# Kernel tuning notes

Measured on AMD Instinct MI355X. Metric: run time of the kernel, lower is better.

Reference implementation:

```python
import jax, jax.numpy as jnp
import numpy as np
from functools import partial

IMG, P, DIM, DEPTH, HEADS, MLP = 224, 16, 768, 6, 12, 3072
N = (IMG // P) ** 2            # 196 patches
PIX = P * P * 3                # 768 pixel values per patch
RATIO = 0.5
NUM_MASKED = int(RATIO * N)    # 98


def patchify(img):
    # b (h p1) (w p2) c -> b (h w) (p1 p2 c)
    b, H, W, c = img.shape
    g = H // P
    x = img.reshape(b, g, P, g, P, c)
    x = x.transpose(0, 1, 3, 2, 4, 5)
    return x.reshape(b, g * g, P * P * c)


def layernorm(x, s, b, eps=1e-5):
    m = jnp.mean(x, axis=-1, keepdims=True)
    v = jnp.var(x, axis=-1, keepdims=True)
    return (x - m) * jax.lax.rsqrt(v + eps) * s + b


def setup_inputs() -> dict:
    key = jax.random.key(0)
    ks = jax.random.split(key, 16)
    B = 64
    s = 0.02
    inp = {
        "img": jax.random.normal(ks[0], (B, IMG, IMG, 3), jnp.float32),
        "mask_noise": jax.random.uniform(ks[1], (B, N), jnp.float32),
        "patch_w": jax.random.normal(ks[2], (PIX, DIM), jnp.float32) * s,
        "patch_b": jnp.zeros((DIM,), jnp.float32),
        "pos_emb": jax.random.normal(ks[3], (1, N + 1, DIM), jnp.float32) * s,
        "mask_token": jax.random.normal(ks[4], (DIM,), jnp.float32),
        "ln1_s": jnp.ones((DEPTH, DIM), jnp.float32),
        "ln1_b": jnp.zeros((DEPTH, DIM), jnp.float32),
        "wqkv": jax.random.normal(ks[5], (DEPTH, DIM, 3 * DIM), jnp.float32) * s,
        "bqkv": jnp.zeros((DEPTH, 3 * DIM), jnp.float32),
        "wo": jax.random.normal(ks[6], (DEPTH, DIM, DIM), jnp.float32) * s,
        "bo": jnp.zeros((DEPTH, DIM), jnp.float32),
        "ln2_s": jnp.ones((DEPTH, DIM), jnp.float32),
        "ln2_b": jnp.zeros((DEPTH, DIM), jnp.float32),
        "w1": jax.random.normal(ks[7], (DEPTH, DIM, MLP), jnp.float32) * s,
        "b1": jnp.zeros((DEPTH, MLP), jnp.float32),
        "w2": jax.random.normal(ks[8], (DEPTH, MLP, DIM), jnp.float32) * s,
        "b2": jnp.zeros((DEPTH, DIM), jnp.float32),
        "pix_w": jax.random.normal(ks[9], (DIM, PIX), jnp.float32) * s,
        "pix_b": jnp.zeros((PIX,), jnp.float32),
    }
    return inp


def transformer(tokens, ln1_s, ln1_b, wqkv, bqkv, wo, bo, ln2_s, ln2_b, w1, b1, w2, b2):
    dh = DIM // HEADS
    scale = 1.0 / jnp.sqrt(jnp.float32(dh))

    def layer(x, p):
        l1s, l1b, Wqkv, Bqkv, Wo, Bo, l2s, l2b, W1, B1, W2, B2 = p
        h = layernorm(x, l1s, l1b)
        qkv = h @ Wqkv + Bqkv                              # [b,n,3D]
        b, n, _ = qkv.shape
        q, k, v = jnp.split(qkv.reshape(b, n, 3, HEADS, dh), 3, axis=2)
        q, k, v = (t[:, :, 0] for t in (q, k, v))          # [b,n,h,d]
        attn = jax.nn.softmax(jnp.einsum('bqhd,bkhd->bhqk', q, k) * scale, axis=-1)
        out = jnp.einsum('bhqk,bkhd->bqhd', attn, v).reshape(b, n, DIM)
        x = x + out @ Wo + Bo
        h = layernorm(x, l2s, l2b)
        x = x + jax.nn.gelu(h @ W1 + B1) @ W2 + B2
        return x, None

    params = (ln1_s, ln1_b, wqkv, bqkv, wo, bo, ln2_s, ln2_b, w1, b1, w2, b2)
    x, _ = jax.lax.scan(layer, tokens, params)
    return x


def reference(img, mask_noise, patch_w, patch_b, pos_emb, mask_token,
              ln1_s, ln1_b, wqkv, bqkv, wo, bo, ln2_s, ln2_b, w1, b1, w2, b2,
              pix_w, pix_b):
    patches = patchify(img)                               # [B,N,PIX]
    B = patches.shape[0]
    batch_range = jnp.arange(B)[:, None]
    pe = pos_emb[:, 1:N + 1]                              # skip cls position

    tokens = patches @ patch_w + patch_b + pe             # [B,N,D]
    mask_tokens = mask_token + pe                         # [1,N,D] broadcast

    _, masked_indices = jax.lax.top_k(mask_noise, NUM_MASKED)   # [B,K]
    bool_mask = jnp.zeros((B, N), bool).at[batch_range, masked_indices].set(True)
    tokens = jnp.where(bool_mask[..., None], mask_tokens, tokens)

    encoded = transformer(tokens, ln1_s, ln1_b, wqkv, bqkv, wo, bo,
                          ln2_s, ln2_b, w1, b1, w2, b2)

    encoded_mask = encoded[batch_range, masked_indices]   # [B,K,D]
    pred = encoded_mask @ pix_w + pix_b                   # [B,K,PIX]
    masked_patches = patches[batch_range, masked_indices]
    recon_loss = jnp.mean(jnp.abs(pred - masked_patches)) / NUM_MASKED
    return recon_loss
```

## Files before the change

kernel.cpp:

```cpp
#include <hip/hip_runtime.h>
#include <hip/hip_bf16.h>
#include <math.h>

#define BATCH   64
#define NPATCH  196
#define DIM     768
#define DEPTH   6
#define HEADS   12
#define DHEAD   64
#define MLPDIM  3072
#define NMASK   98
#define TOKENS  (BATCH*NPATCH)
#define MROWS   (BATCH*NMASK)
#define HALFROWS (TOKENS/2)

using bf16_t = __hip_bfloat16;
typedef short bf16x8 __attribute__((ext_vector_type(8)));
typedef short short4v __attribute__((ext_vector_type(4)));
typedef float floatx4 __attribute__((ext_vector_type(4)));

__device__ inline float gelu_f(float v) {
    const float c = 0.7978845608028654f;
    float t = tanhf(c * (v + 0.044715f * v * v * v));
    return 0.5f * v * (1.0f + t);
}

__device__ __forceinline__ short f2bf_s(float f) {
    bf16_t t = __float2bfloat16(f);
    return *reinterpret_cast<short*>(&t);
}

__device__ __forceinline__ void gload_lds16(const bf16_t* g, bf16_t* l) {
    __builtin_amdgcn_global_load_lds(
        (const __attribute__((address_space(1))) unsigned int*)g,
        (__attribute__((address_space(3))) unsigned int*)l, 16, 0, 0);
}

__device__ __forceinline__ int xcd_swz(int orig, int nwg) {
    const int qq = nwg >> 3, rr = nwg & 7;
    const int xcd = orig & 7, seq = orig >> 3;
    return (xcd < rr ? xcd * (qq + 1) : rr * (qq + 1) + (xcd - rr) * qq) + seq;
}

template<int MODE>
__global__ __launch_bounds__(256) void mm_bf16(
    const bf16_t* __restrict__ A, const bf16_t* __restrict__ BT,
    const float* __restrict__ bias, const float* __restrict__ Cin,
    void* __restrict__ Cout, int M, int N, int K)
{
    __shared__ __align__(16) bf16_t As[128 * 64];
    __shared__ __align__(16) bf16_t Bs[128 * 64];

    const int tid  = threadIdx.x;
    const int lane = tid & 63;
    const int wave = tid >> 6;
    const int wm = (wave >> 1) * 64;
    const int wn = (wave & 1) * 64;

    const int gx  = gridDim.x;
    const int wg = xcd_swz(blockIdx.y * gx + blockIdx.x, gx * gridDim.y);
    const int m0 = (wg / gx) * 128;
    const int n0 = (wg % gx) * 128;

    const int srow = tid >> 3;
    const int schunk = (tid & 7) ^ (srow & 7);
    const bf16_t* gA = A  + (size_t)(m0 + srow) * K + schunk * 8;
    const bf16_t* gB = BT + (size_t)(n0 + srow) * K + schunk * 8;
    bf16_t* lA = &As[tid * 8];
    bf16_t* lB = &Bs[tid * 8];

    floatx4 acc[4][4];
#pragma unroll
    for (int i = 0; i < 4; ++i)
#pragma unroll
        for (int j = 0; j < 4; ++j) acc[i][j] = (floatx4)0.0f;

    const int quad = lane >> 4;
    const int rm = lane & 15;

    for (int k0 = 0; k0 < K; k0 += 64) {
        __syncthreads();
#pragma unroll
        for (int i = 0; i < 4; ++i) {
            gload_lds16(gA + k0 + (size_t)(32 * i) * K, lA + i * 2048);
            gload_lds16(gB + k0 + (size_t)(32 * i) * K, lB + i * 2048);
        }
        __syncthreads();

#pragma unroll
        for (int kk = 0; kk < 2; ++kk) {
            const int kq = (((kk << 2) | quad) ^ (rm & 7)) * 8;
            bf16x8 a[4], b[4];
#pragma unroll
            for (int mi = 0; mi < 4; ++mi)
                a[mi] = *(const bf16x8*)&As[(wm + mi * 16 + rm) * 64 + kq];
#pragma unroll
            for (int ni = 0; ni < 4; ++ni)
                b[ni] = *(const bf16x8*)&Bs[(wn + ni * 16 + rm) * 64 + kq];
#pragma unroll
            for (int mi = 0; mi < 4; ++mi)
#pragma unroll
                for (int ni = 0; ni < 4; ++ni)
                    acc[mi][ni] = __builtin_amdgcn_mfma_f32_16x16x32_bf16(
                        a[mi], b[ni], acc[mi][ni], 0, 0, 0);
        }
    }

    const int cm = m0 + wm + quad * 4;
    const int cn = n0 + wn + rm;
#pragma unroll
    for (int mi = 0; mi < 4; ++mi) {
#pragma unroll
        for (int ni = 0; ni < 4; ++ni) {
#pragma unroll
            for (int r = 0; r < 4; ++r) {
                const int row = cm + mi * 16 + r;
                const int col = cn + ni * 16;
                float v = acc[mi][ni][r] + bias[col];
                const size_t idx = (size_t)row * N + col;
                if (MODE == 0) {
                    ((float*)Cout)[idx] = v;
                } else if (MODE == 1) {
                    ((bf16_t*)Cout)[idx] = __float2bfloat16(gelu_f(v));
                } else if (MODE == 2) {
                    ((float*)Cout)[idx] = v + Cin[idx];
                } else {
                    ((bf16_t*)Cout)[idx] = __float2bfloat16(v);
                }
            }
        }
    }
}

template<int MODE>
__global__ __launch_bounds__(256) void mm64_bf16(
    const bf16_t* __restrict__ A, const bf16_t* __restrict__ BT,
    const float* __restrict__ bias, const float* __restrict__ Cin,
    void* __restrict__ Cout, int M, int N, int K)
{
    __shared__ __align__(16) bf16_t As[64 * 64];
    __shared__ __align__(16) bf16_t Bs[64 * 64];

    const int tid  = threadIdx.x;
    const int lane = tid & 63;
    const int wave = tid >> 6;
    const int wm = (wave >> 1) * 32;
    const int wn = (wave & 1) * 32;

    const int gx  = gridDim.x;
    const int wg = xcd_swz(blockIdx.y * gx + blockIdx.x, gx * gridDim.y);
    const int m0 = (wg / gx) * 64;
    const int n0 = (wg % gx) * 64;

    const int srow = tid >> 3;
    const int schunk = (tid & 7) ^ (srow & 7);
    const bf16_t* gA = A  + (size_t)(m0 + srow) * K + schunk * 8;
    const bf16_t* gB = BT + (size_t)(n0 + srow) * K + schunk * 8;
    bf16_t* lA = &As[tid * 8];
    bf16_t* lB = &Bs[tid * 8];

    floatx4 acc[2][2];
#pragma unroll
    for (int i = 0; i < 2; ++i)
#pragma unroll
        for (int j = 0; j < 2; ++j) acc[i][j] = (floatx4)0.0f;

    const int quad = lane >> 4;
    const int rm = lane & 15;

    for (int k0 = 0; k0 < K; k0 += 64) {
        __syncthreads();
#pragma unroll
        for (int i = 0; i < 2; ++i) {
            gload_lds16(gA + k0 + (size_t)(32 * i) * K, lA + i * 2048);
            gload_lds16(gB + k0 + (size_t)(32 * i) * K, lB + i * 2048);
        }
        __syncthreads();

#pragma unroll
        for (int kk = 0; kk < 2; ++kk) {
            const int kq = (((kk << 2) | quad) ^ (rm & 7)) * 8;
            bf16x8 a[2], b[2];
#pragma unroll
            for (int mi = 0; mi < 2; ++mi)
                a[mi] = *(const bf16x8*)&As[(wm + mi * 16 + rm) * 64 + kq];
#pragma unroll
            for (int ni = 0; ni < 2; ++ni)
                b[ni] = *(const bf16x8*)&Bs[(wn + ni * 16 + rm) * 64 + kq];
#pragma unroll
            for (int mi = 0; mi < 2; ++mi)
#pragma unroll
                for (int ni = 0; ni < 2; ++ni)
                    acc[mi][ni] = __builtin_amdgcn_mfma_f32_16x16x32_bf16(
                        a[mi], b[ni], acc[mi][ni], 0, 0, 0);
        }
    }

    const int cm = m0 + wm + quad * 4;
    const int cn = n0 + wn + rm;
#pragma unroll
    for (int mi = 0; mi < 2; ++mi) {
#pragma unroll
        for (int ni = 0; ni < 2; ++ni) {
#pragma unroll
            for (int r = 0; r < 4; ++r) {
                const int row = cm + mi * 16 + r;
                const int col = cn + ni * 16;
                float v = acc[mi][ni][r] + bias[col];
                const size_t idx = (size_t)row * N + col;
                if (MODE == 0) {
                    ((float*)Cout)[idx] = v;
                } else if (MODE == 1) {
                    ((bf16_t*)Cout)[idx] = __float2bfloat16(gelu_f(v));
                } else if (MODE == 2) {
                    ((float*)Cout)[idx] = v + Cin[idx];
                } else {
                    ((bf16_t*)Cout)[idx] = __float2bfloat16(v);
                }
            }
        }
    }
}

__global__ __launch_bounds__(256) void wconvT(
    const float* __restrict__ W, bf16_t* __restrict__ WT, int K, int N)
{
    __shared__ float t[32][33];
    const size_t off = (size_t)blockIdx.z * K * N;
    const int k0 = blockIdx.y * 32, n0 = blockIdx.x * 32;
    const int r = threadIdx.x >> 5, c = threadIdx.x & 31;
#pragma unroll
    for (int i = 0; i < 4; ++i)
        t[r + i * 8][c] = W[off + (size_t)(k0 + r + i * 8) * N + n0 + c];
    __syncthreads();
#pragma unroll
    for (int i = 0; i < 4; ++i)
        WT[off + (size_t)(n0 + r + i * 8) * K + k0 + c] =
            __float2bfloat16(t[c][r + i * 8]);
}

__global__ __launch_bounds__(256) void patchify_kernel(
    const float* __restrict__ img, bf16_t* __restrict__ patches)
{
    const int row = blockIdx.x;
    const int b = row / NPATCH, p = row % NPATCH;
    const int gy = p / 14, gx = p % 14;
    for (int e = threadIdx.x; e < 768; e += 256) {
        const int c = e % 3, pix = e / 3;
        const int py = pix / 16, px = pix % 16;
        const size_t src = (((size_t)b * 224 + gy * 16 + py) * 224 + gx * 16 + px) * 3 + c;
        patches[(size_t)row * 768 + e] = __float2bfloat16(img[src]);
    }
}

__global__ __launch_bounds__(256) void mask_kernel(
    const float* __restrict__ noise, int* __restrict__ flags, int* __restrict__ midx)
{
    const int b = blockIdx.x;
    __shared__ float v[NPATCH];
    const int t = threadIdx.x;
    if (t < NPATCH) v[t] = noise[b * NPATCH + t];
    __syncthreads();
    if (t < NPATCH) {
        const float mine = v[t];
        int r = 0;
        for (int j = 0; j < NPATCH; ++j) {
            const float o = v[j];
            r += (o > mine) || (o == mine && j < t);
        }
        const int f = (r < NMASK) ? 1 : 0;
        flags[b * NPATCH + t] = f;
        if (f) midx[b * NMASK + r] = t;
    }
}

__global__ __launch_bounds__(256) void pe_mask_kernel(
    float* __restrict__ x, const float* __restrict__ pos_emb,
    const float* __restrict__ mask_token, const int* __restrict__ flags)
{
    const int wave = threadIdx.x >> 6, lane = threadIdx.x & 63;
    const int row = blockIdx.x * 4 + wave;
    const int n = row % NPATCH;
    const int masked = flags[row];
    const float* pe = pos_emb + (size_t)(n + 1) * 768;
    float* xr = x + (size_t)row * 768;
#pragma unroll
    for (int j = 0; j < 3; ++j) {
        const int off = j * 256 + lane * 4;
        const float4 pev = *(const float4*)(pe + off);
        float4 o;
        if (masked) {
            const float4 mt = *(const float4*)(mask_token + off);
            o.x = mt.x + pev.x; o.y = mt.y + pev.y;
            o.z = mt.z + pev.z; o.w = mt.w + pev.w;
        } else {
            const float4 xv = *(const float4*)(xr + off);
            o.x = xv.x + pev.x; o.y = xv.y + pev.y;
            o.z = xv.z + pev.z; o.w = xv.w + pev.w;
        }
        *(float4*)(xr + off) = o;
    }
}

__global__ __launch_bounds__(256) void ln_kernel(
    const float* __restrict__ x, bf16_t* __restrict__ out,
    const float* __restrict__ s, const float* __restrict__ bvec)
{
    const int wave = threadIdx.x >> 6, lane = threadIdx.x & 63;
    const int row = blockIdx.x * 4 + wave;
    const float* xr = x + (size_t)row * 768;

    float4 v[3];
    float sum = 0.0f, sq = 0.0f;
#pragma unroll
    for (int j = 0; j < 3; ++j) {
        v[j] = *(const float4*)(xr + j * 256 + lane * 4);
        sum += v[j].x + v[j].y + v[j].z + v[j].w;
        sq  += v[j].x * v[j].x + v[j].y * v[j].y + v[j].z * v[j].z + v[j].w * v[j].w;
    }
#pragma unroll
    for (int off = 32; off; off >>= 1) {
        sum += __shfl_xor(sum, off, 64);
        sq  += __shfl_xor(sq, off, 64);
    }
    const float mean = sum * (1.0f / 768.0f);
    const float var = sq * (1.0f / 768.0f) - mean * mean;
    const float inv = rsqrtf(var + 1e-5f);

    bf16_t* orow = out + (size_t)row * 768;
#pragma unroll
    for (int j = 0; j < 3; ++j) {
        const int off = j * 256 + lane * 4;
        const float4 sv = *(const float4*)(s + off);
        const float4 bv = *(const float4*)(bvec + off);
        short4v o;
        o[0] = f2bf_s((v[j].x - mean) * inv * sv.x + bv.x);
        o[1] = f2bf_s((v[j].y - mean) * inv * sv.y + bv.y);
        o[2] = f2bf_s((v[j].z - mean) * inv * sv.z + bv.z);
        o[3] = f2bf_s((v[j].w - mean) * inv * sv.w + bv.w);
        *(short4v*)(orow + off) = o;
    }
}

__global__ __launch_bounds__(256) void attn_kernel(
    const bf16_t* __restrict__ qkv, bf16_t* __restrict__ out)
{
    const int bh = blockIdx.x;
    const int b = bh / HEADS, h = bh % HEADS;
    const int tid = threadIdx.x, lane = tid & 63, wave = tid >> 6;
    const int quad = lane >> 4, l16 = lane & 15;
    const int wq = wave * 64;

    __shared__ __align__(16) short Vt[64][68];
    __shared__ __align__(16) short Plds[4][64][68];
    __shared__ float red[4][64];

    const size_t tok0 = (size_t)b * NPATCH;
    const int hoff = h * 64;

    bf16x8 qf[4][2];
#pragma unroll
    for (int ni = 0; ni < 4; ++ni) {
        const int q = wq + ni * 16 + l16;
        const int qe = q < 195 ? q : 195;
#pragma unroll
        for (int ks = 0; ks < 2; ++ks)
            qf[ni][ks] = *(const bf16x8*)(qkv + (tok0 + qe) * 2304 + hoff + ks * 32 + quad * 8);
    }

    floatx4 accO[4][4];
#pragma unroll
    for (int i = 0; i < 4; ++i)
#pragma unroll
        for (int j = 0; j < 4; ++j) accO[i][j] = (floatx4)0.0f;
    float mrun[4], lrun[4];
#pragma unroll
    for (int ni = 0; ni < 4; ++ni) { mrun[ni] = -1e30f; lrun[ni] = 0.0f; }

    for (int kc = 0; kc < 256; kc += 64) {
        __syncthreads();
        {
            const int kl = tid & 63;
            const int dg = tid >> 6;
            const int key = kc + kl;
            if (key < NPATCH) {
                const bf16_t* src = qkv + (tok0 + key) * 2304 + 1536 + hoff + dg * 16;
                bf16x8 v0 = *(const bf16x8*)src;
                bf16x8 v1 = *(const bf16x8*)(src + 8);
#pragma unroll
                for (int j = 0; j < 8; ++j) {
                    Vt[dg * 16 + j][kl]     = v0[j];
                    Vt[dg * 16 + 8 + j][kl] = v1[j];
                }
            } else {
#pragma unroll
                for (int j = 0; j < 16; ++j) Vt[dg * 16 + j][kl] = 0;
            }
        }
        __syncthreads();

        bf16x8 af[4][2];
#pragma unroll
        for (int mi = 0; mi < 4; ++mi) {
            const int key = kc + mi * 16 + l16;
            const int ke = key < 195 ? key : 195;
#pragma unroll
            for (int ks = 0; ks < 2; ++ks)
                af[mi][ks] = *(const bf16x8*)(qkv + (tok0 + ke) * 2304 + 768 + hoff + ks * 32 + quad * 8);
        }
        floatx4 accS[4][4];
#pragma unroll
        for (int i = 0; i < 4; ++i)
#pragma unroll
            for (int j = 0; j < 4; ++j) accS[i][j] = (floatx4)0.0f;
#pragma unroll
        for (int mi = 0; mi < 4; ++mi)
#pragma unroll
            for (int ni = 0; ni < 4; ++ni)
#pragma unroll
                for (int ks = 0; ks < 2; ++ks)
                    accS[mi][ni] = __builtin_amdgcn_mfma_f32_16x16x32_bf16(
                        af[mi][ks], qf[ni][ks], accS[mi][ni], 0, 0, 0);

#pragma unroll
        for (int mi = 0; mi < 4; ++mi) {
#pragma unroll
            for (int r = 0; r < 4; ++r) {
                const int key = kc + mi * 16 + quad * 4 + r;
                const bool valid = key < NPATCH;
#pragma unroll
                for (int ni = 0; ni < 4; ++ni)
                    accS[mi][ni][r] = valid ? accS[mi][ni][r] * 0.125f : -1e30f;
            }
        }

        float alpha[4];
#pragma unroll
        for (int ni = 0; ni < 4; ++ni) {
            float mx = -1e30f;
#pragma unroll
            for (int mi = 0; mi < 4; ++mi)
#pragma unroll
                for (int r = 0; r < 4; ++r) mx = fmaxf(mx, accS[mi][ni][r]);
            mx = fmaxf(mx, __shfl_xor(mx, 16, 64));
            mx = fmaxf(mx, __shfl_xor(mx, 32, 64));
            const float mnew = fmaxf(mrun[ni], mx);
            float s = 0.0f;
#pragma unroll
            for (int mi = 0; mi < 4; ++mi)
#pragma unroll
                for (int r = 0; r < 4; ++r) {
                    const float p = __expf(accS[mi][ni][r] - mnew);
                    accS[mi][ni][r] = p;
                    s += p;
                }
            s += __shfl_xor(s, 16, 64);
            s += __shfl_xor(s, 32, 64);
            alpha[ni] = __expf(mrun[ni] - mnew);
            lrun[ni] = lrun[ni] * alpha[ni] + s;
            mrun[ni] = mnew;
        }
        if (quad == 0) {
#pragma unroll
            for (int ni = 0; ni < 4; ++ni) red[wave][ni * 16 + l16] = alpha[ni];
        }

#pragma unroll
        for (int mi = 0; mi < 4; ++mi)
#pragma unroll
            for (int ni = 0; ni < 4; ++ni) {
                short4v pk;
#pragma unroll
                for (int r = 0; r < 4; ++r) pk[r] = f2bf_s(accS[mi][ni][r]);
                *(short4v*)&Plds[wave][ni * 16 + l16][mi * 16 + quad * 4] = pk;
            }
        asm volatile("s_waitcnt lgkmcnt(0)" ::: "memory");

#pragma unroll
        for (int mi = 0; mi < 4; ++mi) {
            const float4 al = *(const float4*)&red[wave][mi * 16 + quad * 4];
#pragma unroll
            for (int ni = 0; ni < 4; ++ni) {
                accO[mi][ni][0] *= al.x;
                accO[mi][ni][1] *= al.y;
                accO[mi][ni][2] *= al.z;
                accO[mi][ni][3] *= al.w;
            }
        }

#pragma unroll
        for (int ks = 0; ks < 2; ++ks) {
            bf16x8 pa[4], vb[4];
#pragma unroll
            for (int mi = 0; mi < 4; ++mi) {
                short4v lo = *(const short4v*)&Plds[wave][mi * 16 + l16][ks * 32 + quad * 8];
                short4v hi = *(const short4v*)&Plds[wave][mi * 16 + l16][ks * 32 + quad * 8 + 4];
                pa[mi] = __builtin_shufflevector(lo, hi, 0, 1, 2, 3, 4, 5, 6, 7);
            }
#pragma unroll
            for (int ni = 0; ni < 4; ++ni) {
                short4v lo = *(const short4v*)&Vt[ni * 16 + l16][ks * 32 + quad * 8];
                short4v hi = *(const short4v*)&Vt[ni * 16 + l16][ks * 32 + quad * 8 + 4];
                vb[ni] = __builtin_shufflevector(lo, hi, 0, 1, 2, 3, 4, 5, 6, 7);
            }
#pragma unroll
            for (int mi = 0; mi < 4; ++mi)
#pragma unroll
                for (int ni = 0; ni < 4; ++ni)
                    accO[mi][ni] = __builtin_amdgcn_mfma_f32_16x16x32_bf16(
                        pa[mi], vb[ni], accO[mi][ni], 0, 0, 0);
        }
    }

    if (quad == 0) {
#pragma unroll
        for (int ni = 0; ni < 4; ++ni) red[wave][ni * 16 + l16] = lrun[ni];
    }
    asm volatile("s_waitcnt lgkmcnt(0)" ::: "memory");
#pragma unroll
    for (int mi = 0; mi < 4; ++mi) {
        const float4 lv = *(const float4*)&red[wave][mi * 16 + quad * 4];
        const float inv[4] = {1.0f / lv.x, 1.0f / lv.y, 1.0f / lv.z, 1.0f / lv.w};
#pragma unroll
        for (int r = 0; r < 4; ++r) {
            const int q = wq + mi * 16 + quad * 4 + r;
            if (q < NPATCH) {
#pragma unroll
                for (int ni = 0; ni < 4; ++ni) {
                    const int d = ni * 16 + l16;
                    out[(tok0 + q) * 768 + hoff + d] =
                        __float2bfloat16(accO[mi][ni][r] * inv[r]);
                }
            }
        }
    }
}

__global__ __launch_bounds__(256) void gather_kernel(
    const float* __restrict__ x, const int* __restrict__ midx, bf16_t* __restrict__ em)
{
    const int row = blockIdx.x;
    const int b = row / NMASK;
    const int n = midx[row];
    const float* src = x + (size_t)(b * NPATCH + n) * 768;
    bf16_t* dst = em + (size_t)row * 768;
    for (int e = threadIdx.x; e < 768; e += 256) dst[e] = __float2bfloat16(src[e]);
}

__global__ void zero_kernel(float* __restrict__ p) {
    if (threadIdx.x == 0 && blockIdx.x == 0) p[0] = 0.0f;
}

__global__ __launch_bounds__(256) void loss_kernel(
    const float* __restrict__ pred, const float* __restrict__ img,
    const int* __restrict__ midx, float* __restrict__ acc)
{
    const size_t total = (size_t)MROWS * 768;
    float part = 0.0f;
    for (size_t idx = (size_t)blockIdx.x * blockDim.x + threadIdx.x; idx < total;
         idx += (size_t)gridDim.x * blockDim.x) {
        const int e = (int)(idx % 768);
        const int row = (int)(idx / 768);
        const int b = row / NMASK;
        const int n = midx[row];
        const int c = e % 3, pix = e / 3;
        const int py = pix / 16, px = pix % 16;
        const int gy = n / 14, gx = n % 14;
        const float ref =
            img[(((size_t)b * 224 + gy * 16 + py) * 224 + gx * 16 + px) * 3 + c];
        part += fabsf(pred[idx] - ref);
    }
#pragma unroll
    for (int off = 32; off; off >>= 1) part += __shfl_down(part, off, 64);
    __shared__ float sp[4];
    if ((threadIdx.x & 63) == 0) sp[threadIdx.x >> 6] = part;
    __syncthreads();
    if (threadIdx.x == 0) atomicAdd(acc, sp[0] + sp[1] + sp[2] + sp[3]);
}

__global__ void finalize_kernel(const float* __restrict__ acc, float* __restrict__ out)
{
    if (threadIdx.x == 0 && blockIdx.x == 0)
        out[0] = acc[0] * (float)(1.0 / 472055808.0);
}

extern "C" void kernel_launch(void* const* d_in, const int* in_sizes, int n_in,
                              void* d_out, int out_size, void* d_ws, size_t ws_size,
                              hipStream_t stream)
{
    const float* img      = (const float*)d_in[0];
    const float* noise    = (const float*)d_in[1];
    const float* patch_w  = (const float*)d_in[2];
    const float* patch_b  = (const float*)d_in[3];
    const float* pos_emb  = (const float*)d_in[4];
    const float* mask_tok = (const float*)d_in[5];
    const float* ln1_s    = (const float*)d_in[6];
    const float* ln1_b    = (const float*)d_in[7];
    const float* wqkv     = (const float*)d_in[8];
    const float* bqkv     = (const float*)d_in[9];
    const float* wo       = (const float*)d_in[10];
    const float* bo       = (const float*)d_in[11];
    const float* ln2_s    = (const float*)d_in[12];
    const float* ln2_b    = (const float*)d_in[13];
    const float* w1       = (const float*)d_in[14];
    const float* b1       = (const float*)d_in[15];
    const float* w2       = (const float*)d_in[16];
    const float* b2       = (const float*)d_in[17];
    const float* pix_w    = (const float*)d_in[18];
    const float* pix_b    = (const float*)d_in[19];

    const size_t TOK = (size_t)TOKENS * 768;
    float*  x    = (float*)d_ws;
    bf16_t* h    = (bf16_t*)(x + TOK);
    bf16_t* qbuf = h + TOK;
    bf16_t* wts  = qbuf + (size_t)TOKENS * 2304;
    size_t o = 0;
    bf16_t* patch_wT = wts + o; o += (size_t)768 * 768;
    bf16_t* wqkvT    = wts + o; o += (size_t)DEPTH * 2304 * 768;
    bf16_t* woT      = wts + o; o += (size_t)DEPTH * 768 * 768;
    bf16_t* w1T      = wts + o; o += (size_t)DEPTH * 3072 * 768;
    bf16_t* w2T      = wts + o; o += (size_t)DEPTH * 768 * 3072;
    bf16_t* pix_wT   = wts + o; o += (size_t)768 * 768;
    int* flags = (int*)(wts + o);
    int* midx  = flags + TOKENS;
    float* acc = (float*)(midx + MROWS);

    bf16_t* patches = qbuf;
    float*  pred    = (float*)qbuf;

    wconvT<<<dim3(768/32, 768/32, 1), 256, 0, stream>>>(patch_w, patch_wT, 768, 768);
    wconvT<<<dim3(2304/32, 768/32, DEPTH), 256, 0, stream>>>(wqkv, wqkvT, 768, 2304);
    wconvT<<<dim3(768/32, 768/32, DEPTH), 256, 0, stream>>>(wo, woT, 768, 768);
    wconvT<<<dim3(3072/32, 768/32, DEPTH), 256, 0, stream>>>(w1, w1T, 768, 3072);
    wconvT<<<dim3(768/32, 3072/32, DEPTH), 256, 0, stream>>>(w2, w2T, 3072, 768);
    wconvT<<<dim3(768/32, 768/32, 1), 256, 0, stream>>>(pix_w, pix_wT, 768, 768);

    patchify_kernel<<<TOKENS, 256, 0, stream>>>(img, patches);
    mask_kernel<<<BATCH, 256, 0, stream>>>(noise, flags, midx);

    mm64_bf16<0><<<dim3(768/64, TOKENS/64), 256, 0, stream>>>(
        patches, patch_wT, patch_b, nullptr, x, TOKENS, 768, 768);
    pe_mask_kernel<<<TOKENS/4, 256, 0, stream>>>(x, pos_emb, mask_tok, flags);

    for (int l = 0; l < DEPTH; ++l) {
        ln_kernel<<<TOKENS/4, 256, 0, stream>>>(x, h, ln1_s + l * 768, ln1_b + l * 768);
        mm_bf16<3><<<dim3(2304/128, TOKENS/128), 256, 0, stream>>>(
            h, wqkvT + (size_t)l * 2304 * 768, bqkv + l * 2304, nullptr, qbuf,
            TOKENS, 2304, 768);
        attn_kernel<<<BATCH * HEADS, 256, 0, stream>>>(qbuf, h);
        mm64_bf16<2><<<dim3(768/64, TOKENS/64), 256, 0, stream>>>(
            h, woT + (size_t)l * 768 * 768, bo + l * 768, x, x, TOKENS, 768, 768);
        ln_kernel<<<TOKENS/4, 256, 0, stream>>>(x, h, ln2_s + l * 768, ln2_b + l * 768);
        for (int ch = 0; ch < 2; ++ch) {
            bf16_t* hA = h + (size_t)ch * HALFROWS * 768;
            float*  xC = x + (size_t)ch * HALFROWS * 768;
            mm_bf16<1><<<dim3(MLPDIM/128, HALFROWS/128), 256, 0, stream>>>(
                hA, w1T + (size_t)l * 3072 * 768, b1 + l * MLPDIM, nullptr, qbuf,
                HALFROWS, MLPDIM, 768);
            mm64_bf16<2><<<dim3(768/64, HALFROWS/64), 256, 0, stream>>>(
                qbuf, w2T + (size_t)l * 768 * 3072, b2 + l * 768, xC, xC,
                HALFROWS, 768, MLPDIM);
        }
    }

    gather_kernel<<<MROWS, 256, 0, stream>>>(x, midx, h);
    mm64_bf16<0><<<dim3(768/64, MROWS/64), 256, 0, stream>>>(
        h, pix_wT, pix_b, nullptr, pred, MROWS, 768, 768);

    zero_kernel<<<1, 64, 0, stream>>>(acc);
    loss_kernel<<<4704, 256, 0, stream>>>(pred, img, midx, acc);
    finalize_kernel<<<1, 64, 0, stream>>>(acc, (float*)d_out);
}
```

Before: 2.556 ms.

## Double-buffer LDS tiles in 128x128 GEMM and use exp-based tanh in GELU

The 128x128 bf16 GEMM used for QKV and MLP-up now double-buffers its LDS tiles. It issues the global-to-LDS loads for the next K step before running the MFMAs on the current one, which removes one barrier per iteration and overlaps load latency with compute. In exchange, LDS use doubles to 64KB per block, which can lower occupancy. GELU also replaces tanhf with a fast __expf-based tanh, cutting epilogue cost at a small accuracy cost.

```diff
diff --git a/kernel.cpp b/kernel.cpp
--- a/kernel.cpp
+++ b/kernel.cpp
@@ -21,8 +21,12 @@
 
 __device__ inline float gelu_f(float v) {
     const float c = 0.7978845608028654f;
-    float t = tanhf(c * (v + 0.044715f * v * v * v));
-    return 0.5f * v * (1.0f + t);
+    float u = c * (v + 0.044715f * v * v * v);
+    float au = fabsf(u);
+    float e = __expf(-2.0f * au);
+    float th = (1.0f - e) / (1.0f + e);
+    th = copysignf(th, u);
+    return 0.5f * v * (1.0f + th);
 }
 
 __device__ __forceinline__ short f2bf_s(float f) {
@@ -43,13 +47,13 @@
 }
 
 template<int MODE>
-__global__ __launch_bounds__(256) void mm_bf16(
+__global__ __launch_bounds__(256) void mm_db(
     const bf16_t* __restrict__ A, const bf16_t* __restrict__ BT,
     const float* __restrict__ bias, const float* __restrict__ Cin,
     void* __restrict__ Cout, int M, int N, int K)
 {
-    __shared__ __align__(16) bf16_t As[128 * 64];
-    __shared__ __align__(16) bf16_t Bs[128 * 64];
+    __shared__ __align__(16) bf16_t As[2][128 * 64];
+    __shared__ __align__(16) bf16_t Bs[2][128 * 64];
 
     const int tid  = threadIdx.x;
     const int lane = tid & 63;
@@ -66,8 +70,7 @@
     const int schunk = (tid & 7) ^ (srow & 7);
     const bf16_t* gA = A  + (size_t)(m0 + srow) * K + schunk * 8;
     const bf16_t* gB = BT + (size_t)(n0 + srow) * K + schunk * 8;
-    bf16_t* lA = &As[tid * 8];
-    bf16_t* lB = &Bs[tid * 8];
+    const int lds_off = tid * 8;
 
     floatx4 acc[4][4];
 #pragma unroll
@@ -77,15 +80,31 @@
 
     const int quad = lane >> 4;
     const int rm = lane & 15;
-
-    for (int k0 = 0; k0 < K; k0 += 64) {
-        __syncthreads();
-#pragma unroll
-        for (int i = 0; i < 4; ++i) {
-            gload_lds16(gA + k0 + (size_t)(32 * i) * K, lA + i * 2048);
-            gload_lds16(gB + k0 + (size_t)(32 * i) * K, lB + i * 2048);
-        }
-        __syncthreads();
+    const int nt = K >> 6;
+
+#pragma unroll
+    for (int i = 0; i < 4; ++i) {
+        gload_lds16(gA + (size_t)(32 * i) * K, &As[0][lds_off] + i * 2048);
+        gload_lds16(gB + (size_t)(32 * i) * K, &Bs[0][lds_off] + i * 2048);
+    }
+    asm volatile("s_waitcnt vmcnt(0)" ::: "memory");
+    __builtin_amdgcn_s_barrier();
+    asm volatile("" ::: "memory");
+
+    int cur = 0;
+    for (int t = 0; t < nt; ++t) {
+        const bf16_t* sA = cur ? &As[1][0] : &As[0][0];
+        const bf16_t* sB = cur ? &Bs[1][0] : &Bs[0][0];
+        if (t + 1 < nt) {
+            bf16_t* dA = cur ? &As[0][lds_off] : &As[1][lds_off];
+            bf16_t* dB = cur ? &Bs[0][lds_off] : &Bs[1][lds_off];
+            const int koff = (t + 1) * 64;
+#pragma unroll
+            for (int i = 0; i < 4; ++i) {
+                gload_lds16(gA + koff + (size_t)(32 * i) * K, dA + i * 2048);
+                gload_lds16(gB + koff + (size_t)(32 * i) * K, dB + i * 2048);
+            }
+        }
 
 #pragma unroll
         for (int kk = 0; kk < 2; ++kk) {
@@ -93,16 +112,23 @@
             bf16x8 a[4], b[4];
 #pragma unroll
             for (int mi = 0; mi < 4; ++mi)
-                a[mi] = *(const bf16x8*)&As[(wm + mi * 16 + rm) * 64 + kq];
+                a[mi] = *(const bf16x8*)&sA[(wm + mi * 16 + rm) * 64 + kq];
 #pragma unroll
             for (int ni = 0; ni < 4; ++ni)
-                b[ni] = *(const bf16x8*)&Bs[(wn + ni * 16 + rm) * 64 + kq];
+                b[ni] = *(const bf16x8*)&sB[(wn + ni * 16 + rm) * 64 + kq];
 #pragma unroll
             for (int mi = 0; mi < 4; ++mi)
 #pragma unroll
                 for (int ni = 0; ni < 4; ++ni)
                     acc[mi][ni] = __builtin_amdgcn_mfma_f32_16x16x32_bf16(
                         a[mi], b[ni], acc[mi][ni], 0, 0, 0);
+        }
+
+        if (t + 1 < nt) {
+            asm volatile("s_waitcnt vmcnt(0)" ::: "memory");
+            __builtin_amdgcn_s_barrier();
+            asm volatile("" ::: "memory");
+            cur ^= 1;
         }
     }
 
@@ -644,7 +670,7 @@
 
     for (int l = 0; l < DEPTH; ++l) {
         ln_kernel<<<TOKENS/4, 256, 0, stream>>>(x, h, ln1_s + l * 768, ln1_b + l * 768);
-        mm_bf16<3><<<dim3(2304/128, TOKENS/128), 256, 0, stream>>>(
+        mm_db<3><<<dim3(2304/128, TOKENS/128), 256, 0, stream>>>(
             h, wqkvT + (size_t)l * 2304 * 768, bqkv + l * 2304, nullptr, qbuf,
             TOKENS, 2304, 768);
         attn_kernel<<<BATCH * HEADS, 256, 0, stream>>>(qbuf, h);
@@ -654,7 +680,7 @@
         for (int ch = 0; ch < 2; ++ch) {
             bf16_t* hA = h + (size_t)ch * HALFROWS * 768;
             float*  xC = x + (size_t)ch * HALFROWS * 768;
-            mm_bf16<1><<<dim3(MLPDIM/128, HALFROWS/128), 256, 0, stream>>>(
+            mm_db<1><<<dim3(MLPDIM/128, HALFROWS/128), 256, 0, stream>>>(
                 hA, w1T + (size_t)l * 3072 * 768, b1 + l * MLPDIM, nullptr, qbuf,
                 HALFROWS, MLPDIM, 768);
             mm64_bf16<2><<<dim3(768/64, HALFROWS/64), 256, 0, stream>>>(
```

Measured after the change: 2.664 ms. 4.2% more time.
